# Optimization experiments

Hardware: AMD Instinct MI355X
Metric: run time of the kernel (lower is better)

The kernel has to match this reference:

```python
import jax, jax.numpy as jnp
import numpy as np

T, B, DIM, N = 2048, 8, 1024, 64

def setup_inputs() -> dict:
    key = jax.random.key(0)
    ks = jax.random.split(key, 6)
    scale = 1.0 / np.sqrt(DIM)  # xavier-ish for Linear(dim, n_state)
    return {
        "x": jax.random.normal(ks[0], (T, B, DIM), dtype=jnp.float32),
        "S0": jnp.zeros((B, N, N), dtype=jnp.float32),
        "W_k": jax.random.normal(ks[1], (N, DIM), dtype=jnp.float32) * scale,
        "W_v": jax.random.normal(ks[2], (N, DIM), dtype=jnp.float32) * scale,
        "W_q": jax.random.normal(ks[3], (N, DIM), dtype=jnp.float32) * scale,
        "W_alpha": jax.random.normal(ks[4], (N, DIM), dtype=jnp.float32) * scale,
        "b_alpha": jnp.full((N,), 2.0, dtype=jnp.float32),
        "d_g": jnp.full((N,), 0.5, dtype=jnp.float32),
        "b_g": jnp.zeros((N,), dtype=jnp.float32),
    }

def reference(x, S0, W_k, W_v, W_q, W_alpha, b_alpha, d_g, b_g):
    # Precompute all projections: [T, B, N]
    k_all = jnp.einsum('tbd,nd->tbn', x, W_k)
    v_all = jnp.einsum('tbd,nd->tbn', x, W_v)
    q_all = jnp.einsum('tbd,nd->tbn', x, W_q)
    alpha_all = jax.nn.sigmoid(jnp.einsum('tbd,nd->tbn', x, W_alpha) + b_alpha)

    def step(S, inp):
        k, v, q, alpha = inp  # each [B, N]
        retrieved = jnp.einsum('bij,bj->bi', S, k)          # S @ k
        g = jax.nn.sigmoid(d_g * retrieved + b_g)
        v_gated = v * g
        outer_vk = jnp.einsum('bi,bj->bij', v_gated, k)
        S = alpha[..., None] * S + (1.0 - alpha[..., None]) * outer_vk
        out = jnp.einsum('bij,bj->bi', S, q)                # S @ q
        out = out * jax.nn.silu(out)                        # self-gate
        return S, out

    S_final, output = jax.lax.scan(step, S0, (k_all, v_all, q_all, alpha_all))
    return output, S_final
```

## Files before the change

### kernel.cpp

```cpp
#include <hip/hip_runtime.h>

#define TT 2048
#define BB 8
#define DD 1024
#define NN 64
#define C64 64
#define NC2 (TT / C64)

typedef __attribute__((ext_vector_type(8))) short bfrag;
typedef __attribute__((ext_vector_type(4))) float f32x4;
typedef __attribute__((ext_vector_type(8))) unsigned short ushort8;

__device__ __forceinline__ float rcp_(float x) { return __builtin_amdgcn_rcpf(x); }
__device__ __forceinline__ float exp2_(float x) {
#if __has_builtin(__builtin_amdgcn_exp2f)
    return __builtin_amdgcn_exp2f(x);
#else
    return exp2f(x);
#endif
}
__device__ __forceinline__ float sigmoidf_(float x) {
    return rcp_(1.0f + __expf(-x));
}
__device__ __forceinline__ float bcastlane(float x, int l) {
    return __int_as_float(__builtin_amdgcn_readlane(__float_as_int(x), l));
}

template <int CTRL, int RM>
__device__ __forceinline__ float dpp_mul1(float x) {
    int v = __builtin_amdgcn_update_dpp(
        0x3f800000, __float_as_int(x), CTRL, RM, 0xF, false);
    return x * __int_as_float(v);
}
__device__ __forceinline__ float prefix_mul64(float x) {
    x = dpp_mul1<0x111, 0xF>(x);
    x = dpp_mul1<0x112, 0xF>(x);
    x = dpp_mul1<0x114, 0xF>(x);
    x = dpp_mul1<0x118, 0xF>(x);
    x = dpp_mul1<0x142, 0xA>(x);
    x = dpp_mul1<0x143, 0xC>(x);
    return x;
}

__device__ __forceinline__ unsigned short cvt_bf16(float f) {
    unsigned int u = __float_as_uint(f);
    return (unsigned short)((u + 0x7FFF + ((u >> 16) & 1)) >> 16);
}

__device__ __forceinline__ void gll16(const float* g, float* l) {
    __builtin_amdgcn_global_load_lds(
        (const __attribute__((address_space(1))) void*)g,
        (__attribute__((address_space(3))) void*)l, 16, 0, 0);
}

__global__ __launch_bounds__(256) void proj_gemm_kernel(
    const float* __restrict__ x,
    const float* __restrict__ W0, const float* __restrict__ W1,
    const float* __restrict__ W2, const float* __restrict__ W3,
    const float* __restrict__ b_alpha,
    float* __restrict__ O0, float* __restrict__ O1,
    float* __restrict__ O2, float* __restrict__ O3)
{
    const int mat = blockIdx.x;
    const float* __restrict__ W = (mat == 0) ? W0 : (mat == 1) ? W1 : (mat == 2) ? W2 : W3;
    float* __restrict__ C       = (mat == 0) ? O0 : (mat == 1) ? O1 : (mat == 2) ? O2 : O3;

    const int m0   = blockIdx.y * 128;
    const int tid  = threadIdx.x;
    const int lane = tid & 63;
    const int wave = tid >> 6;
    const int ln   = lane & 15;
    const int q8   = (lane >> 4) * 8;

    __shared__ unsigned short As[128][40];
    __shared__ unsigned short Bs[64][40];

    f32x4 acc[2][4] = {};

    const int arow = tid >> 1;
    const int aseg = (tid & 1) * 16;

    float4 pa[4], pb[4];
    {
        const float* ap = &x[(size_t)(m0 + arow) * DD + aseg];
        #pragma unroll
        for (int j = 0; j < 4; j++) pa[j] = *(const float4*)(ap + 4 * j);
        if (tid < 128) {
            const float* bp = &W[(size_t)arow * DD + aseg];
            #pragma unroll
            for (int j = 0; j < 4; j++) pb[j] = *(const float4*)(bp + 4 * j);
        }
    }

    for (int k0 = 0; k0 < DD; k0 += 32) {
        __syncthreads();
        {
            unsigned short t16[16];
            const float* pf = (const float*)pa;
            #pragma unroll
            for (int j = 0; j < 16; j++) t16[j] = cvt_bf16(pf[j]);
            *(ushort8*)&As[arow][aseg]     = *(ushort8*)&t16[0];
            *(ushort8*)&As[arow][aseg + 8] = *(ushort8*)&t16[8];
            if (tid < 128) {
                const float* qf = (const float*)pb;
                #pragma unroll
                for (int j = 0; j < 16; j++) t16[j] = cvt_bf16(qf[j]);
                *(ushort8*)&Bs[arow][aseg]     = *(ushort8*)&t16[0];
                *(ushort8*)&Bs[arow][aseg + 8] = *(ushort8*)&t16[8];
            }
        }
        if (k0 + 32 < DD) {
            const float* ap = &x[(size_t)(m0 + arow) * DD + k0 + 32 + aseg];
            #pragma unroll
            for (int j = 0; j < 4; j++) pa[j] = *(const float4*)(ap + 4 * j);
            if (tid < 128) {
                const float* bp = &W[(size_t)arow * DD + k0 + 32 + aseg];
                #pragma unroll
                for (int j = 0; j < 4; j++) pb[j] = *(const float4*)(bp + 4 * j);
            }
        }
        __syncthreads();

        bfrag af[2], bf[4];
        #pragma unroll
        for (int mt = 0; mt < 2; mt++)
            af[mt] = *(const bfrag*)&As[wave * 32 + mt * 16 + ln][q8];
        #pragma unroll
        for (int nt = 0; nt < 4; nt++)
            bf[nt] = *(const bfrag*)&Bs[nt * 16 + ln][q8];
        #pragma unroll
        for (int mt = 0; mt < 2; mt++)
            #pragma unroll
            for (int nt = 0; nt < 4; nt++)
                acc[mt][nt] = __builtin_amdgcn_mfma_f32_16x16x32_bf16(
                    af[mt], bf[nt], acc[mt][nt], 0, 0, 0);
    }

    #pragma unroll
    for (int nt = 0; nt < 4; nt++) {
        const int col = nt * 16 + ln;
        const float ba = (mat == 3) ? b_alpha[col] : 0.0f;
        #pragma unroll
        for (int mt = 0; mt < 2; mt++) {
            #pragma unroll
            for (int r = 0; r < 4; r++) {
                const int row = m0 + wave * 32 + mt * 16 + (lane >> 4) * 4 + r;
                float v = acc[mt][nt][r];
                if (mat == 3) v = sigmoidf_(v + ba);
                C[(size_t)row * NN + col] = v;
            }
        }
    }
}

__global__ __launch_bounds__(256) void gram_kernel(
    const float* __restrict__ k_all, const float* __restrict__ q_all,
    float* __restrict__ gkq)
{
    const int c  = blockIdx.x;
    const int b  = blockIdx.y;
    const int t0 = c * C64;
    const int tid = threadIdx.x;

    __shared__ __align__(16) float Ks[64][68];
    __shared__ __align__(16) float Qs[64][68];

    {
        const int r = tid >> 2, sg = (tid & 3) * 16;
        const float* kp = &k_all[(size_t)(t0 + r) * (BB * NN) + b * NN + sg];
        const float* qp = &q_all[(size_t)(t0 + r) * (BB * NN) + b * NN + sg];
        #pragma unroll
        for (int j = 0; j < 4; ++j) {
            *(float4*)&Ks[r][sg + 4 * j] = *(const float4*)(kp + 4 * j);
            *(float4*)&Qs[r][sg + 4 * j] = *(const float4*)(qp + 4 * j);
        }
    }
    __syncthreads();

    const int ti = tid >> 4, tj = tid & 15;
    float g[4][4] = {}, kq[4][4] = {};
    #pragma unroll
    for (int c4 = 0; c4 < 16; ++c4) {
        float4 ka[4], kb[4], qb[4];
        #pragma unroll
        for (int r = 0; r < 4; ++r) {
            ka[r] = *(const float4*)&Ks[4 * ti + r][c4 * 4];
            kb[r] = *(const float4*)&Ks[4 * tj + r][c4 * 4];
            qb[r] = *(const float4*)&Qs[4 * tj + r][c4 * 4];
        }
        #pragma unroll
        for (int r = 0; r < 4; ++r)
            #pragma unroll
            for (int q = 0; q < 4; ++q) {
                g[r][q]  = fmaf(ka[r].x, kb[q].x, g[r][q]);
                g[r][q]  = fmaf(ka[r].y, kb[q].y, g[r][q]);
                g[r][q]  = fmaf(ka[r].z, kb[q].z, g[r][q]);
                g[r][q]  = fmaf(ka[r].w, kb[q].w, g[r][q]);
                kq[r][q] = fmaf(ka[r].x, qb[q].x, kq[r][q]);
                kq[r][q] = fmaf(ka[r].y, qb[q].y, kq[r][q]);
                kq[r][q] = fmaf(ka[r].z, qb[q].z, kq[r][q]);
                kq[r][q] = fmaf(ka[r].w, qb[q].w, kq[r][q]);
            }
    }

    float* base = gkq + (size_t)(b * NC2 + c) * 64 * 128;
    #pragma unroll
    for (int r = 0; r < 4; ++r) {
        #pragma unroll
        for (int q = 0; q < 4; ++q) {
            const int t   = 4 * tj + q;
            const int pos = ((ti ^ (t & 15)) << 2) + r;
            base[t * 128 + pos]      = g[r][q];
            base[t * 128 + 64 + pos] = kq[r][q];
        }
    }
}

__global__ __launch_bounds__(256, 1) void scan_kernel(
    const float* __restrict__ gkq,
    const float* __restrict__ k_all, const float* __restrict__ q_all,
    const float* __restrict__ a_all, const float* __restrict__ v_all,
    const float* __restrict__ S0,
    const float* __restrict__ d_g, const float* __restrict__ b_g,
    float* __restrict__ out, float* __restrict__ S_final)
{
    const int b    = blockIdx.x;
    const int rg   = blockIdx.y;
    const int tid  = threadIdx.x;
    const int lane = tid & 63;
    const int wave = tid >> 6;
    const int row  = rg * 4 + wave;

    __shared__ __align__(16) float gT[2][64 * 128];
    __shared__ __align__(16) float Kl[2][64 * 64];
    __shared__ __align__(16) float Ql[2][64 * 64];
    __shared__ __align__(16) float sbuf[4][64];

    float S = S0[((size_t)b * NN + row) * NN + lane];
    const float L2E  = 1.4426950408889634f;
    const float ndg2 = -d_g[row] * L2E;
    const float nbg2 = -b_g[row] * L2E;

    const float* gkq_b = gkq + (size_t)b * NC2 * 64 * 128;

    const int s_loc = lane >> 4;
    const int gr    = lane & 15;

    auto stage = [&](int c, int db) {
        const float* src = gkq_b + (size_t)c * 64 * 128;
        #pragma unroll
        for (int j = 0; j < 8; ++j) {
            const int off = (wave * 16 + 2 * j) * 128;
            gll16(src + off + lane * 4, &gT[db][off]);
        }
        #pragma unroll
        for (int j = 0; j < 4; ++j) {
            const int r0 = wave * 16 + 4 * j;
            const int s  = r0 + s_loc;
            const int gg = gr ^ (s & 15);
            const size_t goff = ((size_t)(c * C64 + s) * BB + b) * NN + gg * 4;
            gll16(k_all + goff, &Kl[db][r0 * 64]);
            gll16(q_all + goff, &Ql[db][r0 * 64]);
        }
    };

    float a_nx, v_nx;
    auto aw_load = [&](int c) {
        const size_t goff = ((size_t)(c * C64 + lane) * BB + b) * NN + row;
        a_nx = a_all[goff];
        v_nx = v_all[goff];
    };

    stage(0, 0);
    aw_load(0);

    for (int c = 0; c < NC2; ++c) {
        const int db = c & 1;
        const float ac = a_nx;
        const float wc = (1.0f - a_nx) * v_nx;
        __syncthreads();
        if (c + 1 < NC2) { aw_load(c + 1); stage(c + 1, db ^ 1); }

        const float P  = prefix_mul64(ac);
        const float Pm = P / ac;
        const float u  = wc * rcp_(P);

        sbuf[wave][lane] = S;
        const float* Kb = &Kl[db][0];
        const float* Qb = &Ql[db][0];
        float4 ha = {0.f, 0.f, 0.f, 0.f};
        float4 hb = {0.f, 0.f, 0.f, 0.f};
        #pragma unroll
        for (int g4 = 0; g4 < 16; ++g4) {
            const int idx = lane * 64 + ((g4 ^ gr) << 2);
            float4 kv = *(const float4*)&Kb[idx];
            float4 qv = *(const float4*)&Qb[idx];
            float4 sv = *(const float4*)&sbuf[wave][g4 << 2];
            ha.x = fmaf(kv.x, sv.x, ha.x); ha.y = fmaf(kv.y, sv.y, ha.y);
            ha.z = fmaf(kv.z, sv.z, ha.z); ha.w = fmaf(kv.w, sv.w, ha.w);
            hb.x = fmaf(qv.x, sv.x, hb.x); hb.y = fmaf(qv.y, sv.y, hb.y);
            hb.z = fmaf(qv.z, sv.z, hb.z); hb.w = fmaf(qv.w, sv.w, hb.w);
        }
        const float h  = (ha.x + ha.y) + (ha.z + ha.w);
        const float hq = (hb.x + hb.y) + (hb.z + hb.w);
        const float e1 = ndg2 * Pm;
        const float e0 = fmaf(e1, h, nbg2);

        float Ga[64], Qa[64];
        {
            const float* gt = &gT[db][0];
            #pragma unroll
            for (int j = 0; j < 16; ++j) {
                const int addr = lane * 128 + ((j ^ gr) << 2);
                const float4 gv = *(const float4*)&gt[addr];
                const float4 qv = *(const float4*)&gt[addr + 64];
                Ga[4 * j + 0] = gv.x; Ga[4 * j + 1] = gv.y;
                Ga[4 * j + 2] = gv.z; Ga[4 * j + 3] = gv.w;
                Qa[4 * j + 0] = qv.x; Qa[4 * j + 1] = qv.y;
                Qa[4 * j + 2] = qv.z; Qa[4 * j + 3] = qv.w;
            }
        }

        float A = 0.f, Bacc = 0.f, Bl = 0.f, chl = 0.f;
        #pragma unroll
        for (int s = 0; s < 64; ++s) {
            const float sg  = rcp_(1.0f + exp2_(fmaf(e1, A, e0)));
            const float s2  = sg * u;
            const float chs = bcastlane(s2, s);
            A    = fmaf(chs, Ga[s], A);
            Bacc = fmaf(chs, Qa[s], Bacc);
            if (lane == s) { Bl = Bacc; chl = chs; }
        }

        float Sa = 0.f;
        #pragma unroll
        for (int s = 0; s < 64; ++s) {
            const float chs = bcastlane(chl, s);
            const float kv  = Kb[s * 64 + (((lane >> 2) ^ (s & 15)) << 2) + (lane & 3)];
            Sa = fmaf(chs, kv, Sa);
        }

        const float o = P * (hq + Bl);
        const float y = o * o * rcp_(1.0f + exp2_(-o * L2E));
        out[((size_t)(c * C64 + lane) * BB + b) * NN + row] = y;
        const float Pl = bcastlane(P, 63);
        S = Pl * (S + Sa);
    }

    S_final[((size_t)b * NN + row) * NN + lane] = S;
}

extern "C" void kernel_launch(void* const* d_in, const int* in_sizes, int n_in,
                              void* d_out, int out_size, void* d_ws, size_t ws_size,
                              hipStream_t stream) {
    const float* x       = (const float*)d_in[0];
    const float* S0      = (const float*)d_in[1];
    const float* W_k     = (const float*)d_in[2];
    const float* W_v     = (const float*)d_in[3];
    const float* W_q     = (const float*)d_in[4];
    const float* W_alpha = (const float*)d_in[5];
    const float* b_alpha = (const float*)d_in[6];
    const float* d_g     = (const float*)d_in[7];
    const float* b_g     = (const float*)d_in[8];
    float* out = (float*)d_out;

    const size_t arr = (size_t)TT * BB * NN;
    float* ws    = (float*)d_ws;
    float* k_all = ws;
    float* v_all = ws + arr;
    float* q_all = ws + 2 * arr;
    float* a_all = ws + 3 * arr;
    float* gkq   = ws + 4 * arr;

    proj_gemm_kernel<<<dim3(4, TT * BB / 128), 256, 0, stream>>>(
        x, W_k, W_v, W_q, W_alpha, b_alpha, k_all, v_all, q_all, a_all);

    gram_kernel<<<dim3(NC2, BB), 256, 0, stream>>>(k_all, q_all, gkq);

    scan_kernel<<<dim3(BB, 16), 256, 0, stream>>>(
        gkq, k_all, q_all, a_all, v_all, S0, d_g, b_g, out, out + arr);
}
```

Before: 326.5 us.

## Fuse four projections into one GEMM pass with pre-converted bf16 weights; split scan finer

```diff
diff --git a/kernel.cpp b/kernel.cpp
--- a/kernel.cpp
+++ b/kernel.cpp
@@ -53,99 +53,111 @@
         (__attribute__((address_space(3))) void*)l, 16, 0, 0);
 }
 
-__global__ __launch_bounds__(256) void proj_gemm_kernel(
-    const float* __restrict__ x,
+__global__ __launch_bounds__(256) void wcvt_kernel(
     const float* __restrict__ W0, const float* __restrict__ W1,
     const float* __restrict__ W2, const float* __restrict__ W3,
+    unsigned short* __restrict__ Wb)
+{
+    const int i = blockIdx.x * 256 + threadIdx.x;
+    const int o = i * 8;
+    const int col = o & 31;
+    const int row = (o >> 5) & 63;
+    const int kt  = (o >> 11) & 31;
+    const int mat = o >> 16;
+    const float* __restrict__ W = (mat == 0) ? W0 : (mat == 1) ? W1
+                                 : (mat == 2) ? W2 : W3;
+    const float* src = &W[(size_t)row * DD + kt * 32 + col];
+    const float4 a = *(const float4*)src;
+    const float4 b = *(const float4*)(src + 4);
+    ushort8 r;
+    r[0] = cvt_bf16(a.x); r[1] = cvt_bf16(a.y);
+    r[2] = cvt_bf16(a.z); r[3] = cvt_bf16(a.w);
+    r[4] = cvt_bf16(b.x); r[5] = cvt_bf16(b.y);
+    r[6] = cvt_bf16(b.z); r[7] = cvt_bf16(b.w);
+    *(ushort8*)&Wb[o] = r;
+}
+
+__global__ __launch_bounds__(256) void proj_fused_kernel(
+    const float* __restrict__ x, const unsigned short* __restrict__ Wb,
     const float* __restrict__ b_alpha,
     float* __restrict__ O0, float* __restrict__ O1,
     float* __restrict__ O2, float* __restrict__ O3)
 {
-    const int mat = blockIdx.x;
-    const float* __restrict__ W = (mat == 0) ? W0 : (mat == 1) ? W1 : (mat == 2) ? W2 : W3;
-    float* __restrict__ C       = (mat == 0) ? O0 : (mat == 1) ? O1 : (mat == 2) ? O2 : O3;
-
-    const int m0   = blockIdx.y * 128;
+    const int m0   = blockIdx.x * 64;
     const int tid  = threadIdx.x;
     const int lane = tid & 63;
     const int wave = tid >> 6;
     const int ln   = lane & 15;
     const int q8   = (lane >> 4) * 8;
 
-    __shared__ unsigned short As[128][40];
-    __shared__ unsigned short Bs[64][40];
-
-    f32x4 acc[2][4] = {};
-
-    const int arow = tid >> 1;
-    const int aseg = (tid & 1) * 16;
-
-    float4 pa[4], pb[4];
+    __shared__ unsigned short As[64][40];
+    __shared__ unsigned short Bs[4][64][40];
+
+    f32x4 acc[4][4] = {};
+
+    const int arow = tid >> 2;
+    const int aseg = (tid & 3) * 8;
+
+    float4 pa[2];
+    ushort8 pw[4];
     {
         const float* ap = &x[(size_t)(m0 + arow) * DD + aseg];
-        #pragma unroll
-        for (int j = 0; j < 4; j++) pa[j] = *(const float4*)(ap + 4 * j);
-        if (tid < 128) {
-            const float* bp = &W[(size_t)arow * DD + aseg];
-            #pragma unroll
-            for (int j = 0; j < 4; j++) pb[j] = *(const float4*)(bp + 4 * j);
-        }
+        pa[0] = *(const float4*)ap;
+        pa[1] = *(const float4*)(ap + 4);
+        const ushort8* wp = (const ushort8*)&Wb[((size_t)(wave * 32 + 0) * 64 + lane) * 32];
+        #pragma unroll
+        for (int j = 0; j < 4; j++) pw[j] = wp[j];
     }
 
     for (int k0 = 0; k0 < DD; k0 += 32) {
         __syncthreads();
         {
-            unsigned short t16[16];
+            unsigned short t8[8];
             const float* pf = (const float*)pa;
             #pragma unroll
-            for (int j = 0; j < 16; j++) t16[j] = cvt_bf16(pf[j]);
-            *(ushort8*)&As[arow][aseg]     = *(ushort8*)&t16[0];
-            *(ushort8*)&As[arow][aseg + 8] = *(ushort8*)&t16[8];
-            if (tid < 128) {
-                const float* qf = (const float*)pb;
-                #pragma unroll
-                for (int j = 0; j < 16; j++) t16[j] = cvt_bf16(qf[j]);
-                *(ushort8*)&Bs[arow][aseg]     = *(ushort8*)&t16[0];
-                *(ushort8*)&Bs[arow][aseg + 8] = *(ushort8*)&t16[8];
-            }
+            for (int j = 0; j < 8; j++) t8[j] = cvt_bf16(pf[j]);
+            *(ushort8*)&As[arow][aseg] = *(ushort8*)&t8[0];
+            #pragma unroll
+            for (int j = 0; j < 4; j++)
+                *(ushort8*)&Bs[wave][lane][8 * j] = pw[j];
         }
         if (k0 + 32 < DD) {
+            const int kt = (k0 >> 5) + 1;
             const float* ap = &x[(size_t)(m0 + arow) * DD + k0 + 32 + aseg];
-            #pragma unroll
-            for (int j = 0; j < 4; j++) pa[j] = *(const float4*)(ap + 4 * j);
-            if (tid < 128) {
-                const float* bp = &W[(size_t)arow * DD + k0 + 32 + aseg];
-                #pragma unroll
-                for (int j = 0; j < 4; j++) pb[j] = *(const float4*)(bp + 4 * j);
-            }
+            pa[0] = *(const float4*)ap;
+            pa[1] = *(const float4*)(ap + 4);
+            const ushort8* wp = (const ushort8*)&Wb[((size_t)(wave * 32 + kt) * 64 + lane) * 32];
+            #pragma unroll
+            for (int j = 0; j < 4; j++) pw[j] = wp[j];
         }
         __syncthreads();
 
-        bfrag af[2], bf[4];
-        #pragma unroll
-        for (int mt = 0; mt < 2; mt++)
-            af[mt] = *(const bfrag*)&As[wave * 32 + mt * 16 + ln][q8];
-        #pragma unroll
-        for (int nt = 0; nt < 4; nt++)
-            bf[nt] = *(const bfrag*)&Bs[nt * 16 + ln][q8];
-        #pragma unroll
-        for (int mt = 0; mt < 2; mt++)
+        const bfrag af = *(const bfrag*)&As[wave * 16 + ln][q8];
+        #pragma unroll
+        for (int mat = 0; mat < 4; mat++) {
+            bfrag bf[4];
             #pragma unroll
             for (int nt = 0; nt < 4; nt++)
-                acc[mt][nt] = __builtin_amdgcn_mfma_f32_16x16x32_bf16(
-                    af[mt], bf[nt], acc[mt][nt], 0, 0, 0);
+                bf[nt] = *(const bfrag*)&Bs[mat][nt * 16 + ln][q8];
+            #pragma unroll
+            for (int nt = 0; nt < 4; nt++)
+                acc[mat][nt] = __builtin_amdgcn_mfma_f32_16x16x32_bf16(
+                    af, bf[nt], acc[mat][nt], 0, 0, 0);
+        }
     }
 
     #pragma unroll
-    for (int nt = 0; nt < 4; nt++) {
-        const int col = nt * 16 + ln;
-        const float ba = (mat == 3) ? b_alpha[col] : 0.0f;
-        #pragma unroll
-        for (int mt = 0; mt < 2; mt++) {
+    for (int mat = 0; mat < 4; mat++) {
+        float* __restrict__ C = (mat == 0) ? O0 : (mat == 1) ? O1
+                               : (mat == 2) ? O2 : O3;
+        #pragma unroll
+        for (int nt = 0; nt < 4; nt++) {
+            const int col = nt * 16 + ln;
+            const float ba = (mat == 3) ? b_alpha[col] : 0.0f;
             #pragma unroll
             for (int r = 0; r < 4; r++) {
-                const int row = m0 + wave * 32 + mt * 16 + (lane >> 4) * 4 + r;
-                float v = acc[mt][nt][r];
+                const int row = m0 + wave * 16 + (lane >> 4) * 4 + r;
+                float v = acc[mat][nt][r];
                 if (mat == 3) v = sigmoidf_(v + ba);
                 C[(size_t)row * NN + col] = v;
             }
@@ -216,7 +228,7 @@
     }
 }
 
-__global__ __launch_bounds__(256, 1) void scan_kernel(
+__global__ __launch_bounds__(128, 1) void scan_kernel(
     const float* __restrict__ gkq,
     const float* __restrict__ k_all, const float* __restrict__ q_all,
     const float* __restrict__ a_all, const float* __restrict__ v_all,
@@ -229,12 +241,12 @@
     const int tid  = threadIdx.x;
     const int lane = tid & 63;
     const int wave = tid >> 6;
-    const int row  = rg * 4 + wave;
+    const int row  = rg * 2 + wave;
 
     __shared__ __align__(16) float gT[2][64 * 128];
     __shared__ __align__(16) float Kl[2][64 * 64];
     __shared__ __align__(16) float Ql[2][64 * 64];
-    __shared__ __align__(16) float sbuf[4][64];
+    __shared__ __align__(16) float sbuf[2][64];
 
     float S = S0[((size_t)b * NN + row) * NN + lane];
     const float L2E  = 1.4426950408889634f;
@@ -249,13 +261,13 @@
     auto stage = [&](int c, int db) {
         const float* src = gkq_b + (size_t)c * 64 * 128;
         #pragma unroll
+        for (int j = 0; j < 16; ++j) {
+            const int off = (wave * 32 + 2 * j) * 128;
+            gll16(src + off + lane * 4, &gT[db][off]);
+        }
+        #pragma unroll
         for (int j = 0; j < 8; ++j) {
-            const int off = (wave * 16 + 2 * j) * 128;
-            gll16(src + off + lane * 4, &gT[db][off]);
-        }
-        #pragma unroll
-        for (int j = 0; j < 4; ++j) {
-            const int r0 = wave * 16 + 4 * j;
+            const int r0 = wave * 32 + 4 * j;
             const int s  = r0 + s_loc;
             const int gg = gr ^ (s & 15);
             const size_t goff = ((size_t)(c * C64 + s) * BB + b) * NN + gg * 4;
@@ -371,12 +383,15 @@
     float* q_all = ws + 2 * arr;
     float* a_all = ws + 3 * arr;
     float* gkq   = ws + 4 * arr;
-
-    proj_gemm_kernel<<<dim3(4, TT * BB / 128), 256, 0, stream>>>(
-        x, W_k, W_v, W_q, W_alpha, b_alpha, k_all, v_all, q_all, a_all);
+    unsigned short* Wb = (unsigned short*)(ws + 6 * arr);
+
+    wcvt_kernel<<<dim3(128), 256, 0, stream>>>(W_k, W_v, W_q, W_alpha, Wb);
+
+    proj_fused_kernel<<<dim3(TT * BB / 64), 256, 0, stream>>>(
+        x, Wb, b_alpha, k_all, v_all, q_all, a_all);
 
     gram_kernel<<<dim3(NC2, BB), 256, 0, stream>>>(k_all, q_all, gkq);
 
-    scan_kernel<<<dim3(BB, 16), 256, 0, stream>>>(
+    scan_kernel<<<dim3(BB, 32), 128, 0, stream>>>(
         gkq, k_all, q_all, a_all, v_all, S0, d_g, b_g, out, out + arr);
 }
```

Result: faster. 320.1 us (-2.0%).
